# Kernel tuning notes

Hardware: AMD Instinct MI355X
Metric: run time of the kernel (lower is better)

Reference implementation:

```python
import jax, jax.numpy as jnp
import numpy as np

B, S, DIN, DOUT = 4, 4096, 4096, 4096
W_SCALE = 0.02  # kaiming-ish scale; keeps values inside fp8 range


def setup_inputs() -> dict:
    key = jax.random.key(0)
    k1, k2, k3 = jax.random.split(key, 3)
    x = jax.random.normal(k1, (B, S, DIN), dtype=jnp.float16)
    weight = (jax.random.normal(k2, (DOUT, DIN), dtype=jnp.float32) * W_SCALE).astype(jnp.float16)
    bias = (jax.random.normal(k3, (DOUT,), dtype=jnp.float32) * W_SCALE).astype(jnp.float16)
    return {"x": x, "weight": weight, "bias": bias}


def reference(x, weight, bias):
    # Emulate torch._scaled_mm: activations quantized to fp8 e5m2,
    # weight (transposed) quantized to fp8 e4m3fn, scale_a = scale_b = 1.0,
    # accumulate in fp32, add fp16 bias, output fp16.
    out_shape = x.shape[:-1] + (weight.shape[0],)
    x8 = x.reshape(-1, x.shape[-1]).astype(jnp.float8_e5m2)       # [M, DIN]
    w8 = weight.T.astype(jnp.float8_e4m3fn)                        # [DIN, DOUT]
    scale = jnp.float32(1.0)  # scale_a * scale_b
    acc = jnp.matmul(x8.astype(jnp.float32), w8.astype(jnp.float32))  # [M, DOUT] fp32 accum
    out = (acc * scale + bias.astype(jnp.float32)).astype(jnp.float16)
    return out.reshape(out_shape)
```

## Files before the change

### kernel.cpp

```cpp
#include <hip/hip_runtime.h>
#include <hip/hip_fp16.h>

#define M_DIM 16384
#define N_DIM 4096
#define K_DIM 4096

typedef __attribute__((ext_vector_type(16))) float f32x16;
typedef __attribute__((ext_vector_type(4)))  int   i32x4;
typedef __attribute__((ext_vector_type(8)))  int   i32x8;

union frag_u { i32x8 v; i32x4 h[2]; };

template<bool E4M3>
__global__ __launch_bounds__(256) void quant_tile_kernel(
    const float* __restrict__ in,
    uint4* __restrict__ out,
    int ngrp)
{
  int t = blockIdx.x * 256 + threadIdx.x;
  if (t >= ngrp) return;
  const int g    = t & 1023;
  const int tile = t >> 10;
  const int kt   = tile & 63;
  const int bt   = tile >> 6;
  const int sb   = g >> 7;
  const int half = (g >> 6) & 1;
  const int l    = g & 63;
  const int row  = bt * 256 + sb * 32 + (l & 31);
  const int k    = kt * 64 + (l >> 5) * 32 + half * 16;

  const float4* p = reinterpret_cast<const float4*>(in + (size_t)row * K_DIM + k);
  float4 v0 = p[0], v1 = p[1], v2 = p[2], v3 = p[3];
  int w0 = 0, w1 = 0, w2 = 0, w3 = 0;
  if (E4M3) {
    w0 = __builtin_amdgcn_cvt_pk_fp8_f32(v0.x, v0.y, w0, false);
    w0 = __builtin_amdgcn_cvt_pk_fp8_f32(v0.z, v0.w, w0, true);
    w1 = __builtin_amdgcn_cvt_pk_fp8_f32(v1.x, v1.y, w1, false);
    w1 = __builtin_amdgcn_cvt_pk_fp8_f32(v1.z, v1.w, w1, true);
    w2 = __builtin_amdgcn_cvt_pk_fp8_f32(v2.x, v2.y, w2, false);
    w2 = __builtin_amdgcn_cvt_pk_fp8_f32(v2.z, v2.w, w2, true);
    w3 = __builtin_amdgcn_cvt_pk_fp8_f32(v3.x, v3.y, w3, false);
    w3 = __builtin_amdgcn_cvt_pk_fp8_f32(v3.z, v3.w, w3, true);
  } else {
    w0 = __builtin_amdgcn_cvt_pk_bf8_f32(v0.x, v0.y, w0, false);
    w0 = __builtin_amdgcn_cvt_pk_bf8_f32(v0.z, v0.w, w0, true);
    w1 = __builtin_amdgcn_cvt_pk_bf8_f32(v1.x, v1.y, w1, false);
    w1 = __builtin_amdgcn_cvt_pk_bf8_f32(v1.z, v1.w, w1, true);
    w2 = __builtin_amdgcn_cvt_pk_bf8_f32(v2.x, v2.y, w2, false);
    w2 = __builtin_amdgcn_cvt_pk_bf8_f32(v2.z, v2.w, w2, true);
    w3 = __builtin_amdgcn_cvt_pk_bf8_f32(v3.x, v3.y, w3, false);
    w3 = __builtin_amdgcn_cvt_pk_bf8_f32(v3.z, v3.w, w3, true);
  }
  out[t] = make_uint4((unsigned)w0, (unsigned)w1, (unsigned)w2, (unsigned)w3);
}

__global__ __launch_bounds__(512, 2) void gemm_fp8_kernel(
    const unsigned char* __restrict__ Aq,
    const unsigned char* __restrict__ Wq,
    const float* __restrict__ bias,
    float* __restrict__ C)
{
  __shared__ __align__(16) unsigned char lds[49152];

  const int tid  = threadIdx.x;
  const int lane = tid & 63;
  const int wave = tid >> 6;
  const int wr   = wave >> 2;
  const int wc   = wave & 3;

  const int bid = blockIdx.x;
  const int swz = (bid & 7) * 128 + (bid >> 3);
  const int bmi = swz >> 4;
  const int bni = swz & 15;

  const unsigned char* tA = Aq + (size_t)bmi * (64 * 16384);
  const unsigned char* tB = Wq + (size_t)bni * (64 * 16384);

  const size_t t16 = (size_t)tid * 16;
  const int    w1k = wave * 1024;
  const unsigned char* gbp = tB + wc * 4096 + lane * 16;

#define STAGE(gb, lo_)                                                      \
  __builtin_amdgcn_global_load_lds(                                        \
      (const __attribute__((address_space(1))) void*)((gb) + t16),          \
      (__attribute__((address_space(3))) void*)(lds + (lo_) + w1k), 16, 0, 0)

#define RD8(dst, off)                                                       \
  { const unsigned char* _p = lds + (off) + lane * 16;                      \
    (dst).h[0] = *reinterpret_cast<const i32x4*>(_p);                       \
    (dst).h[1] = *reinterpret_cast<const i32x4*>(_p + 1024); }

#define LDB(dst, p)                                                         \
  { (dst).h[0] = *reinterpret_cast<const i32x4*>(p);                        \
    (dst).h[1] = *reinterpret_cast<const i32x4*>((p) + 1024); }

#define MFMA(d, a, b)                                                       \
  d = __builtin_amdgcn_mfma_scale_f32_32x32x64_f8f6f4(                      \
      a, b, d, 1 , 0 , 0, 0x7F7F7F7F, 0, 0x7F7F7F7F)

#define SBAR __builtin_amdgcn_sched_barrier(0)
#define BAR  { SBAR; __builtin_amdgcn_s_barrier(); SBAR; }
#define VMW6 { asm volatile("s_waitcnt vmcnt(6)" ::: "memory"); SBAR; }
#define P1   __builtin_amdgcn_s_setprio(1)
#define P0   __builtin_amdgcn_s_setprio(0)

  const int aoff = wr * 8192;

  f32x16 acc[4][2] = {};
  frag_u a0, a1, a2, a3, bE0, bE1, bO0, bO1;

  STAGE(tA, 0); STAGE(tA + 8192, 8192);
  SBAR;
  LDB(bE0, gbp); LDB(bE1, gbp + 2048);
  STAGE(tA + 16384, 16384); STAGE(tA + 24576, 24576);
  SBAR;
  VMW6;
  BAR;

  int cA = 0, cB = 16384, cC = 32768;

  for (int it = 0; it < 32; ++it) {
    const int t = it << 1;
    {
      const size_t tpB = (size_t)((t + 1) & 63) * 16384;
      const size_t tpA = (size_t)((t + 2) & 63) * 16384;
      LDB(bO0, gbp + tpB); LDB(bO1, gbp + tpB + 2048);
      STAGE(tA + tpA, cC); STAGE(tA + tpA + 8192, cC + 8192);
      SBAR;
      RD8(a0, cA + aoff);        RD8(a1, cA + aoff + 2048);
      RD8(a2, cA + aoff + 4096); RD8(a3, cA + aoff + 6144);
      P1;
      MFMA(acc[0][0], a0.v, bE0.v); MFMA(acc[0][1], a0.v, bE1.v);
      MFMA(acc[1][0], a1.v, bE0.v); MFMA(acc[1][1], a1.v, bE1.v);
      MFMA(acc[2][0], a2.v, bE0.v); MFMA(acc[2][1], a2.v, bE1.v);
      MFMA(acc[3][0], a3.v, bE0.v); MFMA(acc[3][1], a3.v, bE1.v);
      P0;
      VMW6;
      BAR;
    }
    {
      const size_t tpB = (size_t)((t + 2) & 63) * 16384;
      const size_t tpA = (size_t)((t + 3) & 63) * 16384;
      LDB(bE0, gbp + tpB); LDB(bE1, gbp + tpB + 2048);
      STAGE(tA + tpA, cA); STAGE(tA + tpA + 8192, cA + 8192);
      SBAR;
      RD8(a0, cB + aoff);        RD8(a1, cB + aoff + 2048);
      RD8(a2, cB + aoff + 4096); RD8(a3, cB + aoff + 6144);
      P1;
      MFMA(acc[0][0], a0.v, bO0.v); MFMA(acc[0][1], a0.v, bO1.v);
      MFMA(acc[1][0], a1.v, bO0.v); MFMA(acc[1][1], a1.v, bO1.v);
      MFMA(acc[2][0], a2.v, bO0.v); MFMA(acc[2][1], a2.v, bO1.v);
      MFMA(acc[3][0], a3.v, bO0.v); MFMA(acc[3][1], a3.v, bO1.v);
      P0;
      VMW6;
      BAR;
    }
    const int nA = cC, nB = cA, nC = cB;
    cA = nA; cB = nB; cC = nC;
  }
#undef STAGE
#undef RD8
#undef LDB
#undef MFMA
#undef SBAR
#undef BAR
#undef VMW6
#undef P1
#undef P0

  #pragma unroll
  for (int n = 0; n < 2; ++n) {
    const int col = bni * 256 + wc * 64 + n * 32 + (lane & 31);
    const float bv = bias[col];
    #pragma unroll
    for (int m = 0; m < 4; ++m) {
      const int rbase = bmi * 256 + wr * 128 + m * 32 + ((lane >> 5) << 2);
      #pragma unroll
      for (int r = 0; r < 16; ++r) {
        const int row = rbase + (r & 3) + 8 * (r >> 2);
        C[(size_t)row * N_DIM + col] =
            __half2float(__float2half_rn(acc[m][n][r] + bv));
      }
    }
  }
}

extern "C" void kernel_launch(void* const* d_in, const int* in_sizes, int n_in,
                              void* d_out, int out_size, void* d_ws, size_t ws_size,
                              hipStream_t stream) {
  const float* x  = (const float*)d_in[0];
  const float* w  = (const float*)d_in[1];
  const float* bs = (const float*)d_in[2];
  float* out = (float*)d_out;

  unsigned char* xq = (unsigned char*)d_ws;
  unsigned char* wq = (unsigned char*)d_ws + (size_t)M_DIM * K_DIM;

  const int ngx = (M_DIM * K_DIM) / 16;
  const int ngw = (N_DIM * K_DIM) / 16;
  quant_tile_kernel<false><<<ngx / 256, 256, 0, stream>>>(x, (uint4*)xq, ngx);
  quant_tile_kernel<true ><<<ngw / 256, 256, 0, stream>>>(w, (uint4*)wq, ngw);

  gemm_fp8_kernel<<<1024, 512, 0, stream>>>(xq, wq, bs, out);
}
```

Before: 411.8 us.

## Stage both A and B tiles through LDS with 4-deep ring and register double-buffering

Replaces direct global loads of B fragments into registers with global_load_lds staging of both A and B tiles into a four-buffer 128KB LDS ring. Fragments for the next tile are read from LDS into an alternate register set while MFMAs run on the current one, and prefetch depth rises to three tiles ahead. The aim is to hide global latency and remove per-wave redundant B loads from global memory. In exchange, 128KB of LDS per block likely drops occupancy from two blocks per CU to one, and the register count grows.

```diff
diff --git a/kernel.cpp b/kernel.cpp
--- a/kernel.cpp
+++ b/kernel.cpp
@@ -60,7 +60,7 @@
     const float* __restrict__ bias,
     float* __restrict__ C)
 {
-  __shared__ __align__(16) unsigned char lds[49152];
+  __shared__ __align__(16) unsigned char lds[131072];
 
   const int tid  = threadIdx.x;
   const int lane = tid & 63;
@@ -78,93 +78,91 @@
 
   const size_t t16 = (size_t)tid * 16;
   const int    w1k = wave * 1024;
-  const unsigned char* gbp = tB + wc * 4096 + lane * 16;
 
 #define STAGE(gb, lo_)                                                      \
   __builtin_amdgcn_global_load_lds(                                        \
       (const __attribute__((address_space(1))) void*)((gb) + t16),          \
       (__attribute__((address_space(3))) void*)(lds + (lo_) + w1k), 16, 0, 0)
 
+#define STAGE_TILE(tp, base)                                                \
+  STAGE(tA + (tp), (base));          STAGE(tA + (tp) + 8192, (base) + 8192); \
+  STAGE(tB + (tp), (base) + 16384);  STAGE(tB + (tp) + 8192, (base) + 24576)
+
 #define RD8(dst, off)                                                       \
   { const unsigned char* _p = lds + (off) + lane * 16;                      \
     (dst).h[0] = *reinterpret_cast<const i32x4*>(_p);                       \
     (dst).h[1] = *reinterpret_cast<const i32x4*>(_p + 1024); }
 
-#define LDB(dst, p)                                                         \
-  { (dst).h[0] = *reinterpret_cast<const i32x4*>(p);                        \
-    (dst).h[1] = *reinterpret_cast<const i32x4*>((p) + 1024); }
-
 #define MFMA(d, a, b)                                                       \
   d = __builtin_amdgcn_mfma_scale_f32_32x32x64_f8f6f4(                      \
       a, b, d, 1 , 0 , 0, 0x7F7F7F7F, 0, 0x7F7F7F7F)
 
 #define SBAR __builtin_amdgcn_sched_barrier(0)
-#define BAR  { SBAR; __builtin_amdgcn_s_barrier(); SBAR; }
-#define VMW6 { asm volatile("s_waitcnt vmcnt(6)" ::: "memory"); SBAR; }
 #define P1   __builtin_amdgcn_s_setprio(1)
 #define P0   __builtin_amdgcn_s_setprio(0)
 
   const int aoff = wr * 8192;
+  const int boff = 16384 + wc * 4096;
 
   f32x16 acc[4][2] = {};
-  frag_u a0, a1, a2, a3, bE0, bE1, bO0, bO1;
-
-  STAGE(tA, 0); STAGE(tA + 8192, 8192);
-  SBAR;
-  LDB(bE0, gbp); LDB(bE1, gbp + 2048);
-  STAGE(tA + 16384, 16384); STAGE(tA + 24576, 24576);
-  SBAR;
-  VMW6;
-  BAR;
-
-  int cA = 0, cB = 16384, cC = 32768;
-
-  for (int it = 0; it < 32; ++it) {
-    const int t = it << 1;
-    {
-      const size_t tpB = (size_t)((t + 1) & 63) * 16384;
-      const size_t tpA = (size_t)((t + 2) & 63) * 16384;
-      LDB(bO0, gbp + tpB); LDB(bO1, gbp + tpB + 2048);
-      STAGE(tA + tpA, cC); STAGE(tA + tpA + 8192, cC + 8192);
-      SBAR;
-      RD8(a0, cA + aoff);        RD8(a1, cA + aoff + 2048);
-      RD8(a2, cA + aoff + 4096); RD8(a3, cA + aoff + 6144);
-      P1;
-      MFMA(acc[0][0], a0.v, bE0.v); MFMA(acc[0][1], a0.v, bE1.v);
-      MFMA(acc[1][0], a1.v, bE0.v); MFMA(acc[1][1], a1.v, bE1.v);
-      MFMA(acc[2][0], a2.v, bE0.v); MFMA(acc[2][1], a2.v, bE1.v);
-      MFMA(acc[3][0], a3.v, bE0.v); MFMA(acc[3][1], a3.v, bE1.v);
-      P0;
-      VMW6;
-      BAR;
-    }
-    {
-      const size_t tpB = (size_t)((t + 2) & 63) * 16384;
-      const size_t tpA = (size_t)((t + 3) & 63) * 16384;
-      LDB(bE0, gbp + tpB); LDB(bE1, gbp + tpB + 2048);
-      STAGE(tA + tpA, cA); STAGE(tA + tpA + 8192, cA + 8192);
-      SBAR;
-      RD8(a0, cB + aoff);        RD8(a1, cB + aoff + 2048);
-      RD8(a2, cB + aoff + 4096); RD8(a3, cB + aoff + 6144);
-      P1;
-      MFMA(acc[0][0], a0.v, bO0.v); MFMA(acc[0][1], a0.v, bO1.v);
-      MFMA(acc[1][0], a1.v, bO0.v); MFMA(acc[1][1], a1.v, bO1.v);
-      MFMA(acc[2][0], a2.v, bO0.v); MFMA(acc[2][1], a2.v, bO1.v);
-      MFMA(acc[3][0], a3.v, bO0.v); MFMA(acc[3][1], a3.v, bO1.v);
-      P0;
-      VMW6;
-      BAR;
-    }
-    const int nA = cC, nB = cA, nC = cB;
-    cA = nA; cB = nB; cC = nC;
+  frag_u Ea0, Ea1, Ea2, Ea3, Eb0, Eb1;
+  frag_u Oa0, Oa1, Oa2, Oa3, Ob0, Ob1;
+
+#define RDTILE(s, buf)                                                      \
+  RD8(s##a0, (buf) + aoff);        RD8(s##a1, (buf) + aoff + 2048);         \
+  RD8(s##a2, (buf) + aoff + 4096); RD8(s##a3, (buf) + aoff + 6144);         \
+  RD8(s##b0, (buf) + boff);        RD8(s##b1, (buf) + boff + 2048)
+
+#define TILE_STEP(rdset, mfset, rdbuf, stbuf, tp3)                          \
+  SBAR;                                                                     \
+  RDTILE(rdset, rdbuf);                                                     \
+  SBAR;                                                                     \
+  P1;                                                                       \
+  MFMA(acc[0][0], mfset##a0.v, mfset##b0.v);                                \
+  MFMA(acc[0][1], mfset##a0.v, mfset##b1.v);                                \
+  MFMA(acc[1][0], mfset##a1.v, mfset##b0.v);                                \
+  MFMA(acc[1][1], mfset##a1.v, mfset##b1.v);                                \
+  MFMA(acc[2][0], mfset##a2.v, mfset##b0.v);                                \
+  MFMA(acc[2][1], mfset##a2.v, mfset##b1.v);                                \
+  MFMA(acc[3][0], mfset##a3.v, mfset##b0.v);                                \
+  MFMA(acc[3][1], mfset##a3.v, mfset##b1.v);                                \
+  P0;                                                                       \
+  SBAR;                                                                     \
+  STAGE_TILE(tp3, stbuf);                                                   \
+  SBAR;                                                                     \
+  asm volatile("s_waitcnt vmcnt(4)" ::: "memory");                          \
+  SBAR;                                                                     \
+  __builtin_amdgcn_s_barrier()
+
+  STAGE_TILE(0, 0);
+  STAGE_TILE(16384, 32768);
+  STAGE_TILE(32768, 65536);
+  SBAR;
+  asm volatile("s_waitcnt vmcnt(4)" ::: "memory");
+  SBAR;
+  __builtin_amdgcn_s_barrier();
+  SBAR;
+  RDTILE(E, 0);
+  SBAR;
+
+  for (int it = 0; it < 16; ++it) {
+    const int t = it << 2;
+    const size_t tp3 = (size_t)((t + 3) & 63) * 16384;
+    const size_t tp4 = (size_t)((t + 4) & 63) * 16384;
+    const size_t tp5 = (size_t)((t + 5) & 63) * 16384;
+    const size_t tp6 = (size_t)((t + 6) & 63) * 16384;
+    TILE_STEP(O, E, 32768, 98304, tp3);
+    TILE_STEP(E, O, 65536, 0, tp4);
+    TILE_STEP(O, E, 98304, 32768, tp5);
+    TILE_STEP(E, O, 0, 65536, tp6);
   }
 #undef STAGE
+#undef STAGE_TILE
 #undef RD8
-#undef LDB
+#undef RDTILE
 #undef MFMA
+#undef TILE_STEP
 #undef SBAR
-#undef BAR
-#undef VMW6
 #undef P1
 #undef P0
 
```

Result: faster. 352.9 us (-14.3%).
